# Kernel optimization log

Measured on AMD Instinct MI355X. Metric: run time of the kernel, lower is better.

The kernel has to match this reference:

```python
import jax, jax.numpy as jnp
import numpy as np

NUM_USERS = 50000
NUM_ITEMS = 50000
EMB_K = 8
N = 8192
GAMMA = 0.1


def setup_inputs() -> dict:
    key = jax.random.key(0)
    ks = jax.random.split(key, 11)
    s = 1.0
    return {
        "x": jax.random.randint(ks[0], (N, 2), 0, NUM_ITEMS, dtype=jnp.int64) if jax.config.jax_enable_x64 else jax.random.randint(ks[0], (N, 2), 0, NUM_ITEMS),
        "y": jax.random.randint(ks[1], (N, 2), 0, NUM_ITEMS),
        "W": jax.random.normal(ks[2], (NUM_USERS, EMB_K), jnp.float32) * s,
        "H": jax.random.normal(ks[3], (NUM_ITEMS, EMB_K), jnp.float32) * s,
        "ncf_user_emb": jax.random.normal(ks[4], (NUM_USERS, EMB_K), jnp.float32) * s,
        "ncf_item_emb": jax.random.normal(ks[5], (NUM_ITEMS, EMB_K), jnp.float32) * s,
        "lin1_w": jax.random.normal(ks[6], (EMB_K, 2 * EMB_K), jnp.float32) * 0.1,
        "lin1_b": jax.random.normal(ks[7], (EMB_K,), jnp.float32) * 0.1,
        "lin2_w": jax.random.normal(ks[8], (1, EMB_K), jnp.float32) * 0.1,
        "mf_user_emb": jax.random.normal(ks[9], (NUM_USERS, EMB_K), jnp.float32) * s,
        "mf_item_emb": jax.random.normal(ks[10], (NUM_ITEMS, EMB_K), jnp.float32) * s,
    }


def _get_embedding(idx, Wt, Ht):
    # concat user/item embeddings -> [N, 2k], then the (buggy, faithful) min/max step
    feat = jnp.concatenate([Wt[idx[:, 0]], Ht[idx[:, 1]]], axis=1)
    f_min = jnp.min(feat)
    f_max = jnp.max(feat)
    feat = feat - f_min / (f_max - f_min)  # scalar division binds first, as in source
    return feat / feat.shape[1]


def _exp_kernel(X, Y, gamma):
    # Euclidean cdist(Y, X) via gram trick (no [Ny,Nx,d] intermediate), then exp(-d*gamma)
    d2 = (jnp.sum(Y * Y, axis=1)[:, None]
          + jnp.sum(X * X, axis=1)[None, :]
          - 2.0 * (Y @ X.T))
    d = jnp.sqrt(jnp.maximum(d2, 0.0))
    return jnp.exp(-d * gamma)


def reference(x, y, W, H, ncf_user_emb, ncf_item_emb, lin1_w, lin1_b, lin2_w, mf_user_emb, mf_item_emb):
    # kernel branch
    fx = _get_embedding(x, W, H)  # [N, 2k]
    fy = _get_embedding(y, W, H)  # [N, 2k]
    K = _exp_kernel(fx, fy, GAMMA)  # [Ny, Nx]
    # NCF prediction model on x
    ue = ncf_user_emb[x[:, 0]]
    ie = ncf_item_emb[x[:, 1]]
    z = jnp.concatenate([ue, ie], axis=1)
    h1 = jax.nn.relu(z @ lin1_w.T + lin1_b)
    pred = h1 @ lin2_w.T  # [N, 1]
    # MF weight model on x
    mu = mf_user_emb[x[:, 0]]
    mi = mf_item_emb[x[:, 1]]
    w = jnp.sum(mu * mi, axis=1, keepdims=True)  # [N, 1]
    return (K, pred, w)
```

## Files before the change

kernel.cpp:

```cpp
#include <hip/hip_runtime.h>

#define NN 8192
#define GAMMA 0.1f

typedef float v2f __attribute__((ext_vector_type(2)));
typedef float v4f __attribute__((ext_vector_type(4)));

__global__ __launch_bounds__(256) void prep_kernel(
    const int* __restrict__ x, const int* __restrict__ y,
    const float* __restrict__ W, const float* __restrict__ H,
    const float* __restrict__ nue, const float* __restrict__ nie,
    const float* __restrict__ l1w, const float* __restrict__ l1b,
    const float* __restrict__ l2w,
    const float* __restrict__ mfu, const float* __restrict__ mfi,
    float* __restrict__ pred, float* __restrict__ wout,
    float* __restrict__ pmn, float* __restrict__ pmx)
{
    int gid = blockIdx.x * 256 + threadIdx.x;
    bool isx = gid < NN;
    int i = isx ? gid : gid - NN;
    const int* idx = isx ? x : y;
    int iu = idx[2 * i], iv = idx[2 * i + 1];

    const float4* wp = (const float4*)(W + (size_t)iu * 8);
    float4 w0 = wp[0], w1 = wp[1];
    const float4* hp = (const float4*)(H + (size_t)iv * 8);
    float4 h0 = hp[0], h1 = hp[1];

    float f[16];
    f[0] = w0.x; f[1] = w0.y; f[2] = w0.z; f[3] = w0.w;
    f[4] = w1.x; f[5] = w1.y; f[6] = w1.z; f[7] = w1.w;
    f[8] = h0.x; f[9] = h0.y; f[10] = h0.z; f[11] = h0.w;
    f[12] = h1.x; f[13] = h1.y; f[14] = h1.z; f[15] = h1.w;

    float mn = f[0], mx = f[0];
#pragma unroll
    for (int k = 1; k < 16; k++) { mn = fminf(mn, f[k]); mx = fmaxf(mx, f[k]); }
#pragma unroll
    for (int off = 1; off < 64; off <<= 1) {
        mn = fminf(mn, __shfl_xor(mn, off));
        mx = fmaxf(mx, __shfl_xor(mx, off));
    }
    if ((threadIdx.x & 63) == 0) {
        int wid = gid >> 6;
        pmn[wid] = mn;
        pmx[wid] = mx;
    }

    if (isx) {
        const float4* up = (const float4*)(nue + (size_t)iu * 8);
        float4 u0 = up[0], u1 = up[1];
        const float4* ip = (const float4*)(nie + (size_t)iv * 8);
        float4 i0 = ip[0], i1 = ip[1];
        float z[16];
        z[0] = u0.x; z[1] = u0.y; z[2] = u0.z; z[3] = u0.w;
        z[4] = u1.x; z[5] = u1.y; z[6] = u1.z; z[7] = u1.w;
        z[8] = i0.x; z[9] = i0.y; z[10] = i0.z; z[11] = i0.w;
        z[12] = i1.x; z[13] = i1.y; z[14] = i1.z; z[15] = i1.w;

        float p = 0.f;
#pragma unroll
        for (int k = 0; k < 8; k++) {
            float h = l1b[k];
#pragma unroll
            for (int m = 0; m < 16; m++) h = fmaf(z[m], l1w[k * 16 + m], h);
            h = fmaxf(h, 0.f);
            p = fmaf(h, l2w[k], p);
        }
        pred[i] = p;

        const float4* ap = (const float4*)(mfu + (size_t)iu * 8);
        float4 a0 = ap[0], a1 = ap[1];
        const float4* bp = (const float4*)(mfi + (size_t)iv * 8);
        float4 b0 = bp[0], b1 = bp[1];
        float wv = a0.x * b0.x + a0.y * b0.y + a0.z * b0.z + a0.w * b0.w
                 + a1.x * b1.x + a1.y * b1.y + a1.z * b1.z + a1.w * b1.w;
        wout[i] = wv;
    }
}

__global__ __launch_bounds__(256) void norm_kernel(
    const int* __restrict__ x, const int* __restrict__ y,
    const float* __restrict__ W, const float* __restrict__ H,
    const float* __restrict__ pmn, const float* __restrict__ pmx,
    float* __restrict__ fxs, float* __restrict__ fyn,
    float* __restrict__ nx, float* __restrict__ ny)
{
    __shared__ float red[256];
    int tid = threadIdx.x;
    int gid = blockIdx.x * 256 + tid;
    bool isx = gid < NN;
    int side = isx ? 0 : 1;

    if (tid < 128) red[tid] = pmn[side * 128 + tid];
    else           red[tid] = pmx[side * 128 + (tid - 128)];
    __syncthreads();
#pragma unroll
    for (int s = 64; s >= 1; s >>= 1) {
        if ((tid & 127) < s) {
            float o = red[tid + s];
            red[tid] = (tid < 128) ? fminf(red[tid], o) : fmaxf(red[tid], o);
        }
        __syncthreads();
    }
    float fmn = red[0], fmx = red[128];
    float c = fmn / (fmx - fmn);

    int i = isx ? gid : gid - NN;
    const int* idx = isx ? x : y;
    int iu = idx[2 * i], iv = idx[2 * i + 1];
    const float4* wp = (const float4*)(W + (size_t)iu * 8);
    float4 w0 = wp[0], w1 = wp[1];
    const float4* hp = (const float4*)(H + (size_t)iv * 8);
    float4 h0 = hp[0], h1 = hp[1];

    float f[16];
    f[0] = w0.x; f[1] = w0.y; f[2] = w0.z; f[3] = w0.w;
    f[4] = w1.x; f[5] = w1.y; f[6] = w1.z; f[7] = w1.w;
    f[8] = h0.x; f[9] = h0.y; f[10] = h0.z; f[11] = h0.w;
    f[12] = h1.x; f[13] = h1.y; f[14] = h1.z; f[15] = h1.w;

    float g[16];
    float s = 0.f;
    float sc2 = isx ? -2.f : 1.f;
    float o[16];
#pragma unroll
    for (int k = 0; k < 16; k++) {
        g[k] = (f[k] - c) * (1.f / 16.f);
        s = fmaf(g[k], g[k], s);
        o[k] = g[k] * sc2;
    }
    float* dst = (isx ? fxs : fyn) + (size_t)i * 16;
    float4* dv = (float4*)dst;
    dv[0] = make_float4(o[0], o[1], o[2], o[3]);
    dv[1] = make_float4(o[4], o[5], o[6], o[7]);
    dv[2] = make_float4(o[8], o[9], o[10], o[11]);
    dv[3] = make_float4(o[12], o[13], o[14], o[15]);
    (isx ? nx : ny)[i] = s;
}

__global__ __launch_bounds__(256) void kexp_kernel(
    const float* __restrict__ fxs, const float* __restrict__ fyn,
    const float* __restrict__ nx, const float* __restrict__ ny,
    float* __restrict__ K)
{
    __shared__ float sfy[512];
    __shared__ float sny[32];
    int tid = threadIdx.x;
    int ib = blockIdx.y * 32;
    int jb = blockIdx.x * 1024;

    for (int t = tid; t < 512; t += 256) sfy[t] = fyn[(size_t)ib * 16 + t];
    if (tid < 32) sny[tid] = ny[ib + tid];
    __syncthreads();

    int j0 = jb + tid * 4;
    v2f a[4][8];
    float nxr[4];
#pragma unroll
    for (int c2 = 0; c2 < 4; c2++) {
        const float4* p = (const float4*)(fxs + (size_t)(j0 + c2) * 16);
        float4 v0 = p[0], v1 = p[1], v2 = p[2], v3 = p[3];
        a[c2][0] = (v2f){v0.x, v0.y}; a[c2][1] = (v2f){v0.z, v0.w};
        a[c2][2] = (v2f){v1.x, v1.y}; a[c2][3] = (v2f){v1.z, v1.w};
        a[c2][4] = (v2f){v2.x, v2.y}; a[c2][5] = (v2f){v2.z, v2.w};
        a[c2][6] = (v2f){v3.x, v3.y}; a[c2][7] = (v2f){v3.z, v3.w};
        nxr[c2] = nx[j0 + c2];
    }

    const float4* sfy4 = (const float4*)sfy;
    const float CC = 2.0813689894397856e-2f;

#pragma unroll 2
    for (int i = 0; i < 32; i++) {
        float4 q0 = sfy4[i * 4 + 0], q1 = sfy4[i * 4 + 1];
        float4 q2 = sfy4[i * 4 + 2], q3 = sfy4[i * 4 + 3];
        v2f fy[8];
        fy[0] = (v2f){q0.x, q0.y}; fy[1] = (v2f){q0.z, q0.w};
        fy[2] = (v2f){q1.x, q1.y}; fy[3] = (v2f){q1.z, q1.w};
        fy[4] = (v2f){q2.x, q2.y}; fy[5] = (v2f){q2.z, q2.w};
        fy[6] = (v2f){q3.x, q3.y}; fy[7] = (v2f){q3.z, q3.w};
        float nyv = sny[i];
        float r[4];
#pragma unroll
        for (int c2 = 0; c2 < 4; c2++) {
            v2f acc = (v2f){nyv + nxr[c2], 0.f};
#pragma unroll
            for (int k = 0; k < 8; k++)
                acc = __builtin_elementwise_fma(a[c2][k], fy[k], acc);
            float d2 = fmaxf(acc.x + acc.y, 0.f);
            r[c2] = __builtin_amdgcn_exp2f(-__builtin_amdgcn_sqrtf(d2 * CC));
        }
        v4f o = (v4f){r[0], r[1], r[2], r[3]};
        __builtin_nontemporal_store(o, (v4f*)(K + (size_t)(ib + i) * NN + j0));
    }
}

extern "C" void kernel_launch(void* const* d_in, const int* in_sizes, int n_in,
                              void* d_out, int out_size, void* d_ws, size_t ws_size,
                              hipStream_t stream) {
    const int* x = (const int*)d_in[0];
    const int* y = (const int*)d_in[1];
    const float* W = (const float*)d_in[2];
    const float* H = (const float*)d_in[3];
    const float* nue = (const float*)d_in[4];
    const float* nie = (const float*)d_in[5];
    const float* l1w = (const float*)d_in[6];
    const float* l1b = (const float*)d_in[7];
    const float* l2w = (const float*)d_in[8];
    const float* mfu = (const float*)d_in[9];
    const float* mfi = (const float*)d_in[10];

    float* out = (float*)d_out;
    float* K = out;
    float* pred = out + (size_t)NN * NN;
    float* wout = pred + NN;

    float* pmn = (float*)d_ws;
    float* pmx = pmn + 256;
    float* fxs = pmx + 256;
    float* fyn = fxs + (size_t)NN * 16;
    float* nx  = fyn + (size_t)NN * 16;
    float* ny  = nx + NN;

    hipLaunchKernelGGL(prep_kernel, dim3(64), dim3(256), 0, stream,
                       x, y, W, H, nue, nie, l1w, l1b, l2w, mfu, mfi, pred, wout, pmn, pmx);
    hipLaunchKernelGGL(norm_kernel, dim3(64), dim3(256), 0, stream,
                       x, y, W, H, pmn, pmx, fxs, fyn, nx, ny);
    hipLaunchKernelGGL(kexp_kernel, dim3(8, 256), dim3(256), 0, stream,
                       fxs, fyn, nx, ny, K);
}
```

Before: 60.24 us.

## Fuse normalization into kexp kernel, dropping norm launch and workspace round-trip

Removes the separate norm_kernel. Each kexp block now reduces the per-wave min/max partials itself, gathers and normalizes its own 32 y rows into shared memory and its 4 x rows into registers. The gamma/log2 constant is folded into the y features and norms, so the inner loop skips one multiply. This saves a kernel launch and the fxs/fyn global write/read, at the cost of redundant gathers and min/max reductions across the 2048 blocks.

```diff
diff --git a/kernel.cpp b/kernel.cpp
--- a/kernel.cpp
+++ b/kernel.cpp
@@ -79,97 +79,98 @@
     }
 }
 
-__global__ __launch_bounds__(256) void norm_kernel(
+__global__ __launch_bounds__(256) void kexp_kernel(
     const int* __restrict__ x, const int* __restrict__ y,
     const float* __restrict__ W, const float* __restrict__ H,
     const float* __restrict__ pmn, const float* __restrict__ pmx,
-    float* __restrict__ fxs, float* __restrict__ fyn,
-    float* __restrict__ nx, float* __restrict__ ny)
-{
-    __shared__ float red[256];
-    int tid = threadIdx.x;
-    int gid = blockIdx.x * 256 + tid;
-    bool isx = gid < NN;
-    int side = isx ? 0 : 1;
-
-    if (tid < 128) red[tid] = pmn[side * 128 + tid];
-    else           red[tid] = pmx[side * 128 + (tid - 128)];
-    __syncthreads();
-#pragma unroll
-    for (int s = 64; s >= 1; s >>= 1) {
-        if ((tid & 127) < s) {
-            float o = red[tid + s];
-            red[tid] = (tid < 128) ? fminf(red[tid], o) : fmaxf(red[tid], o);
-        }
-        __syncthreads();
-    }
-    float fmn = red[0], fmx = red[128];
-    float c = fmn / (fmx - fmn);
-
-    int i = isx ? gid : gid - NN;
-    const int* idx = isx ? x : y;
-    int iu = idx[2 * i], iv = idx[2 * i + 1];
-    const float4* wp = (const float4*)(W + (size_t)iu * 8);
-    float4 w0 = wp[0], w1 = wp[1];
-    const float4* hp = (const float4*)(H + (size_t)iv * 8);
-    float4 h0 = hp[0], h1 = hp[1];
-
-    float f[16];
-    f[0] = w0.x; f[1] = w0.y; f[2] = w0.z; f[3] = w0.w;
-    f[4] = w1.x; f[5] = w1.y; f[6] = w1.z; f[7] = w1.w;
-    f[8] = h0.x; f[9] = h0.y; f[10] = h0.z; f[11] = h0.w;
-    f[12] = h1.x; f[13] = h1.y; f[14] = h1.z; f[15] = h1.w;
-
-    float g[16];
-    float s = 0.f;
-    float sc2 = isx ? -2.f : 1.f;
-    float o[16];
-#pragma unroll
-    for (int k = 0; k < 16; k++) {
-        g[k] = (f[k] - c) * (1.f / 16.f);
-        s = fmaf(g[k], g[k], s);
-        o[k] = g[k] * sc2;
-    }
-    float* dst = (isx ? fxs : fyn) + (size_t)i * 16;
-    float4* dv = (float4*)dst;
-    dv[0] = make_float4(o[0], o[1], o[2], o[3]);
-    dv[1] = make_float4(o[4], o[5], o[6], o[7]);
-    dv[2] = make_float4(o[8], o[9], o[10], o[11]);
-    dv[3] = make_float4(o[12], o[13], o[14], o[15]);
-    (isx ? nx : ny)[i] = s;
-}
-
-__global__ __launch_bounds__(256) void kexp_kernel(
-    const float* __restrict__ fxs, const float* __restrict__ fyn,
-    const float* __restrict__ nx, const float* __restrict__ ny,
     float* __restrict__ K)
 {
     __shared__ float sfy[512];
     __shared__ float sny[32];
+    __shared__ float sred[4];
     int tid = threadIdx.x;
     int ib = blockIdx.y * 32;
     int jb = blockIdx.x * 1024;
-
-    for (int t = tid; t < 512; t += 256) sfy[t] = fyn[(size_t)ib * 16 + t];
-    if (tid < 32) sny[tid] = ny[ib + tid];
+    const float CC = 2.0813689894397856e-2f;
+
+    {
+        int wv = tid >> 6, ln = tid & 63;
+        const float* psrc = (wv & 1) ? pmx : pmn;
+        int base = (wv >> 1) * 128;
+        float u0 = psrc[base + ln], u1 = psrc[base + ln + 64];
+        float v = (wv & 1) ? fmaxf(u0, u1) : fminf(u0, u1);
+#pragma unroll
+        for (int off = 1; off < 64; off <<= 1) {
+            float o = __shfl_xor(v, off);
+            v = (wv & 1) ? fmaxf(v, o) : fminf(v, o);
+        }
+        if (ln == 0) sred[wv] = v;
+    }
     __syncthreads();
+    float cx = sred[0] / (sred[1] - sred[0]);
+    float cy = sred[2] / (sred[3] - sred[2]);
+
+    if (tid < 32) {
+        int r = ib + tid;
+        int iu = y[2 * r], iv = y[2 * r + 1];
+        const float4* wp = (const float4*)(W + (size_t)iu * 8);
+        float4 w0 = wp[0], w1 = wp[1];
+        const float4* hp = (const float4*)(H + (size_t)iv * 8);
+        float4 h0 = hp[0], h1 = hp[1];
+        float f[16];
+        f[0] = w0.x; f[1] = w0.y; f[2] = w0.z; f[3] = w0.w;
+        f[4] = w1.x; f[5] = w1.y; f[6] = w1.z; f[7] = w1.w;
+        f[8] = h0.x; f[9] = h0.y; f[10] = h0.z; f[11] = h0.w;
+        f[12] = h1.x; f[13] = h1.y; f[14] = h1.z; f[15] = h1.w;
+        float s = 0.f;
+        float g[16];
+#pragma unroll
+        for (int k = 0; k < 16; k++) {
+            g[k] = (f[k] - cy) * (1.f / 16.f);
+            s = fmaf(g[k], g[k], s);
+        }
+        float4* dv = (float4*)(sfy + tid * 16);
+        dv[0] = make_float4(g[0] * CC, g[1] * CC, g[2] * CC, g[3] * CC);
+        dv[1] = make_float4(g[4] * CC, g[5] * CC, g[6] * CC, g[7] * CC);
+        dv[2] = make_float4(g[8] * CC, g[9] * CC, g[10] * CC, g[11] * CC);
+        dv[3] = make_float4(g[12] * CC, g[13] * CC, g[14] * CC, g[15] * CC);
+        sny[tid] = s * CC;
+    }
 
     int j0 = jb + tid * 4;
     v2f a[4][8];
     float nxr[4];
-#pragma unroll
-    for (int c2 = 0; c2 < 4; c2++) {
-        const float4* p = (const float4*)(fxs + (size_t)(j0 + c2) * 16);
-        float4 v0 = p[0], v1 = p[1], v2 = p[2], v3 = p[3];
-        a[c2][0] = (v2f){v0.x, v0.y}; a[c2][1] = (v2f){v0.z, v0.w};
-        a[c2][2] = (v2f){v1.x, v1.y}; a[c2][3] = (v2f){v1.z, v1.w};
-        a[c2][4] = (v2f){v2.x, v2.y}; a[c2][5] = (v2f){v2.z, v2.w};
-        a[c2][6] = (v2f){v3.x, v3.y}; a[c2][7] = (v2f){v3.z, v3.w};
-        nxr[c2] = nx[j0 + c2];
-    }
+    {
+        int4 xi0 = *(const int4*)(x + 2 * j0);
+        int4 xi1 = *(const int4*)(x + 2 * j0 + 4);
+        int iu[4] = {xi0.x, xi0.z, xi1.x, xi1.z};
+        int iv[4] = {xi0.y, xi0.w, xi1.y, xi1.w};
+#pragma unroll
+        for (int c = 0; c < 4; c++) {
+            const float4* wp = (const float4*)(W + (size_t)iu[c] * 8);
+            float4 w0 = wp[0], w1 = wp[1];
+            const float4* hp = (const float4*)(H + (size_t)iv[c] * 8);
+            float4 h0 = hp[0], h1 = hp[1];
+            float f[16];
+            f[0] = w0.x; f[1] = w0.y; f[2] = w0.z; f[3] = w0.w;
+            f[4] = w1.x; f[5] = w1.y; f[6] = w1.z; f[7] = w1.w;
+            f[8] = h0.x; f[9] = h0.y; f[10] = h0.z; f[11] = h0.w;
+            f[12] = h1.x; f[13] = h1.y; f[14] = h1.z; f[15] = h1.w;
+            float s = 0.f;
+#pragma unroll
+            for (int k = 0; k < 8; k++) {
+                float g0 = (f[2 * k] - cx) * (1.f / 16.f);
+                float g1 = (f[2 * k + 1] - cx) * (1.f / 16.f);
+                s = fmaf(g0, g0, s);
+                s = fmaf(g1, g1, s);
+                a[c][k] = (v2f){-2.f * g0, -2.f * g1};
+            }
+            nxr[c] = s * CC;
+        }
+    }
+    __syncthreads();
 
     const float4* sfy4 = (const float4*)sfy;
-    const float CC = 2.0813689894397856e-2f;
 
 #pragma unroll 2
     for (int i = 0; i < 32; i++) {
@@ -189,7 +190,7 @@
             for (int k = 0; k < 8; k++)
                 acc = __builtin_elementwise_fma(a[c2][k], fy[k], acc);
             float d2 = fmaxf(acc.x + acc.y, 0.f);
-            r[c2] = __builtin_amdgcn_exp2f(-__builtin_amdgcn_sqrtf(d2 * CC));
+            r[c2] = __builtin_amdgcn_exp2f(-__builtin_amdgcn_sqrtf(d2));
         }
         v4f o = (v4f){r[0], r[1], r[2], r[3]};
         __builtin_nontemporal_store(o, (v4f*)(K + (size_t)(ib + i) * NN + j0));
@@ -218,15 +219,9 @@
 
     float* pmn = (float*)d_ws;
     float* pmx = pmn + 256;
-    float* fxs = pmx + 256;
-    float* fyn = fxs + (size_t)NN * 16;
-    float* nx  = fyn + (size_t)NN * 16;
-    float* ny  = nx + NN;
 
     hipLaunchKernelGGL(prep_kernel, dim3(64), dim3(256), 0, stream,
                        x, y, W, H, nue, nie, l1w, l1b, l2w, mfu, mfi, pred, wout, pmn, pmx);
-    hipLaunchKernelGGL(norm_kernel, dim3(64), dim3(256), 0, stream,
-                       x, y, W, H, pmn, pmx, fxs, fyn, nx, ny);
     hipLaunchKernelGGL(kexp_kernel, dim3(8, 256), dim3(256), 0, stream,
-                       fxs, fyn, nx, ny, K);
+                       x, y, W, H, pmn, pmx, K);
 }
```

New measurement: 63.04 us. 1.05x slower.
